# Kernel optimization log

Hardware: AMD Instinct MI355X
Metric: run time of the kernel (lower is better)

Reference implementation:

```python
import jax, jax.numpy as jnp
import numpy as np

N_EMBD = 1024
N_HEAD = 16
B, T = 4, 2048


def setup_inputs() -> dict:
    key = jax.random.key(0)
    ks = jax.random.split(key, 4)
    s = 1.0 / np.sqrt(N_EMBD)
    return {
        "x": jax.random.normal(ks[0], (B, T, N_EMBD), dtype=jnp.float32),
        "w_attn": jax.random.normal(ks[1], (N_EMBD, 3 * N_EMBD), dtype=jnp.float32) * s,
        "b_attn": jnp.zeros((3 * N_EMBD,), dtype=jnp.float32),
        "w_proj": jax.random.normal(ks[2], (N_EMBD, N_EMBD), dtype=jnp.float32) * s,
        "b_proj": jnp.zeros((N_EMBD,), dtype=jnp.float32),
    }


def reference(x, w_attn, b_attn, w_proj, b_proj):
    Bb, Tt, C = x.shape
    H = N_HEAD
    D = C // H  # head dim
    qkv = x @ w_attn + b_attn  # [B,T,3C]
    q, k, v = jnp.split(qkv, 3, axis=2)
    # [B,H,T,D]
    q = q.reshape(Bb, Tt, H, D).transpose(0, 2, 1, 3)
    k = k.reshape(Bb, Tt, H, D).transpose(0, 2, 1, 3)
    v = v.reshape(Bb, Tt, H, D).transpose(0, 2, 1, 3)
    scale = 1.0 / np.sqrt(D).astype(np.float32)
    attn = jnp.einsum("bhqd,bhkd->bhqk", q, k) * scale
    mask = jnp.tril(jnp.ones((Tt, Tt), dtype=bool))
    attn = jnp.where(mask, attn, jnp.float32(-jnp.inf))
    probs = jax.nn.softmax(attn, axis=-1)
    out = jnp.einsum("bhqk,bhkd->bhqd", probs, v)
    out = out.transpose(0, 2, 1, 3).reshape(Bb, Tt, C)
    return out @ w_proj + b_proj
```

## Files before the change

### kernel.cpp

```cpp
#include <hip/hip_runtime.h>
#include <hip/hip_bf16.h>


typedef float f32x4 __attribute__((ext_vector_type(4)));
typedef float f32x16 __attribute__((ext_vector_type(16)));
typedef short short8 __attribute__((ext_vector_type(8)));
typedef short short4v __attribute__((ext_vector_type(4)));

__device__ __forceinline__ short f2bf(float f) {
  union { __hip_bfloat16 h; short s; } u;
  u.h = __float2bfloat16(f);
  return u.s;
}

__device__ __forceinline__ void gl_lds16(const void* g, void* l) {
  __builtin_amdgcn_global_load_lds(
      (const __attribute__((address_space(1))) void*)g,
      (__attribute__((address_space(3))) void*)l, 16, 0, 0);
}

__global__ void prep(const float* __restrict__ x, const float* __restrict__ wa,
                     const float* __restrict__ wp, short* __restrict__ xb,
                     short* __restrict__ wat, short* __restrict__ wpt) {
  const int bid = blockIdx.x, tid = threadIdx.x;
  if (bid < 8192) {
    int i = (bid * 256 + tid) * 4;
    float4 v = *(const float4*)(x + i);
    short4v o;
    o[0] = f2bf(v.x); o[1] = f2bf(v.y); o[2] = f2bf(v.z); o[3] = f2bf(v.w);
    *(short4v*)(xb + i) = o;
    return;
  }
  __shared__ float tile[32][33];
  const float* in;
  short* out;
  int N, bx, by;
  if (bid < 11264) {
    int t = bid - 8192;
    in = wa; out = wat; N = 3072; bx = t % 96; by = t / 96;
  } else {
    int t = bid - 11264;
    in = wp; out = wpt; N = 1024; bx = t & 31; by = t >> 5;
  }
  int tx = tid & 31, ty = tid >> 5;
  int x0 = bx * 32, y0 = by * 32;
#pragma unroll
  for (int i = 0; i < 32; i += 8)
    tile[ty + i][tx] = in[(size_t)(y0 + ty + i) * N + x0 + tx];
  __syncthreads();
#pragma unroll
  for (int i = 0; i < 32; i += 8)
    out[(size_t)(x0 + ty + i) * 1024 + y0 + tx] = f2bf(tile[tx][ty + i]);
}


#define GEMM_BODY(A_, Bt_)                                                        \
  __shared__ __align__(16) short As[2][128 * 32];                                 \
  __shared__ __align__(16) short Bs[2][128 * 32];                                 \
  const int tid = threadIdx.x;                                                    \
  const int wv = tid >> 6;                                                        \
  const int wr = wv >> 1, wc = wv & 1;                                            \
  const int col = tid & 31, khalf = (tid >> 5) & 1;                               \
  const int m0 = blockIdx.y * 128, n0 = blockIdx.x * 128;                         \
  const int cc0 = tid, cc1 = tid + 256;                                           \
  const int row0 = cc0 >> 2, part0 = ((cc0 & 3) - ((cc0 >> 3) & 3)) & 3;          \
  const int row1 = cc1 >> 2, part1 = ((cc1 & 3) - ((cc1 >> 3) & 3)) & 3;          \
  const size_t ga0 = (size_t)(m0 + row0) * 1024 + part0 * 8;                      \
  const size_t ga1 = (size_t)(m0 + row1) * 1024 + part1 * 8;                      \
  const size_t gb0 = (size_t)(n0 + row0) * 1024 + part0 * 8;                      \
  const size_t gb1 = (size_t)(n0 + row1) * 1024 + part1 * 8;                      \
  f32x16 acc[2][2];                                                               \
  _Pragma("unroll") for (int i = 0; i < 2; ++i)                                   \
      _Pragma("unroll") for (int j = 0; j < 2; ++j)                               \
          acc[i][j] = (f32x16)(0.f);                                              \
  gl_lds16(A_ + ga0, (char*)As[0] + cc0 * 16);                                    \
  gl_lds16(A_ + ga1, (char*)As[0] + cc1 * 16);                                    \
  gl_lds16(Bt_ + gb0, (char*)Bs[0] + cc0 * 16);                                   \
  gl_lds16(Bt_ + gb1, (char*)Bs[0] + cc1 * 16);                                   \
  __syncthreads();                                                                \
  for (int kt = 0; kt < 32; ++kt) {                                               \
    if (kt + 1 < 32) {                                                            \
      const int k0 = (kt + 1) * 32;                                               \
      char* Ad = (char*)As[(kt + 1) & 1];                                         \
      char* Bd = (char*)Bs[(kt + 1) & 1];                                         \
      gl_lds16(A_ + ga0 + k0, Ad + cc0 * 16);                                     \
      gl_lds16(A_ + ga1 + k0, Ad + cc1 * 16);                                     \
      gl_lds16(Bt_ + gb0 + k0, Bd + cc0 * 16);                                    \
      gl_lds16(Bt_ + gb1 + k0, Bd + cc1 * 16);                                    \
    }                                                                             \
    const short* Ac = As[kt & 1];                                                 \
    const short* Bc = Bs[kt & 1];                                                 \
    short8 af[2][2], bf[2][2];                                                    \
    _Pragma("unroll") for (int i = 0; i < 2; ++i)                                 \
        _Pragma("unroll") for (int s = 0; s < 2; ++s) {                           \
          int pa = s * 2 + khalf;                                                 \
          int ra = wr * 64 + i * 32 + col;                                        \
          int rb = wc * 64 + i * 32 + col;                                        \
          af[i][s] = *(const short8*)&Ac[(ra * 4 + ((pa + (ra >> 1)) & 3)) * 8];  \
          bf[i][s] = *(const short8*)&Bc[(rb * 4 + ((pa + (rb >> 1)) & 3)) * 8];  \
        }                                                                         \
    _Pragma("unroll") for (int s = 0; s < 2; ++s)                                 \
        _Pragma("unroll") for (int i = 0; i < 2; ++i)                             \
            _Pragma("unroll") for (int j = 0; j < 2; ++j)                         \
                acc[i][j] = __builtin_amdgcn_mfma_f32_32x32x16_bf16(              \
                    af[i][s], bf[j][s], acc[i][j], 0, 0, 0);                      \
    __syncthreads();                                                              \
  }

__global__ __launch_bounds__(256, 2) void gemm_qkv(
    const short* __restrict__ A, const short* __restrict__ Bt,
    const float* __restrict__ bias, short* __restrict__ Qb,
    short* __restrict__ Kb, short* __restrict__ Vtb) {
  GEMM_BODY(A, Bt)
  const int rhalf = khalf * 4;
#pragma unroll
  for (int i = 0; i < 2; ++i) {
#pragma unroll
    for (int j = 0; j < 2; ++j) {
      int n = n0 + wc * 64 + j * 32 + col;
      int n2 = n & 1023;
      int hh = n2 >> 6, d = n2 & 63;
      float bv = bias[n];
      int mb = m0 + wr * 64 + i * 32 + rhalf;
      int bb = mb >> 11;
      int bh = (bb << 4) + hh;
      if (n < 2048) {
        const bool isq = n < 1024;
#pragma unroll
        for (int a = 0; a < 16; ++a) {
          int t = (mb + (a & 3) + 8 * (a >> 2)) & 2047;
          float o = acc[i][j][a] + bv;
          size_t idx = ((size_t)bh * 2048 + t) * 64 + d;
          if (isq)
            Qb[idx] = f2bf(o * 0.18033688f);
          else
            Kb[idx] = f2bf(o);
        }
      } else {
#pragma unroll
        for (int g = 0; g < 4; ++g) {
          int t = (mb + 8 * g) & 2047;
          short4v o;
#pragma unroll
          for (int r = 0; r < 4; ++r) o[r] = f2bf(acc[i][j][g * 4 + r] + bv);
          *(short4v*)&Vtb[((size_t)bh * 64 + d) * 2048 + t] = o;
        }
      }
    }
  }
}

__global__ __launch_bounds__(256, 2) void gemm_proj(
    const short* __restrict__ A, const short* __restrict__ Bt,
    const float* __restrict__ bias, float* __restrict__ out) {
  GEMM_BODY(A, Bt)
  const int rhalf = khalf * 4;
#pragma unroll
  for (int i = 0; i < 2; ++i) {
#pragma unroll
    for (int j = 0; j < 2; ++j) {
      int n = n0 + wc * 64 + j * 32 + col;
      float bv = bias[n];
      int mb = m0 + wr * 64 + i * 32 + rhalf;
#pragma unroll
      for (int a = 0; a < 16; ++a) {
        int m = mb + (a & 3) + 8 * (a >> 2);
        out[(size_t)m * 1024 + n] = acc[i][j][a] + bv;
      }
    }
  }
}

__global__ __launch_bounds__(256, 2) void flash_attn(
    const short* __restrict__ Qg_, const short* __restrict__ Kg_,
    const short* __restrict__ Vg_, short* __restrict__ Ob) {
  constexpr int STR = 72;
  __shared__ __align__(16) short Kl[2][64 * STR];
  __shared__ __align__(16) short Vl[2][64 * STR];
  const int tid = threadIdx.x;
  const int wv = tid >> 6, ln = tid & 15, quad = (tid & 63) >> 4;
  const int bh = blockIdx.x & 63;
  const int pair = blockIdx.x >> 6;
  const short* Qg = Qg_ + (size_t)bh * 2048 * 64;
  const short* Kg = Kg_ + (size_t)bh * 2048 * 64;
  const short* Vg = Vg_ + (size_t)bh * 64 * 2048;
  const int srow = tid >> 3, spart = tid & 7;
  const int bb = bh >> 4, hh = bh & 15;

  short8 kreg[2], vreg[2];

#define LOADKV(KT)                                                              \
  {                                                                             \
    const short* Kt = Kg + (size_t)(KT) * 64 * 64;                              \
    _Pragma("unroll") for (int i = 0; i < 2; ++i) {                             \
      kreg[i] = *(const short8*)(Kt + (size_t)(srow + i * 32) * 64 + spart * 8);\
      vreg[i] = *(const short8*)(Vg + (size_t)(srow + i * 32) * 2048 +          \
                                 (KT) * 64 + spart * 8);                        \
    }                                                                           \
  }
#define WRITEKV(BUF)                                                            \
  _Pragma("unroll") for (int i = 0; i < 2; ++i) {                               \
    *(short8*)&Kl[BUF][(srow + i * 32) * STR + spart * 8] = kreg[i];            \
    *(short8*)&Vl[BUF][(srow + i * 32) * STR + spart * 8] = vreg[i];            \
  }

#pragma unroll
  for (int it = 0; it < 2; ++it) {
    const int qt = it ? pair : (15 - pair);
    const int q0 = qt * 128;
    const int qbase = q0 + wv * 32;
    const int nkt = (q0 >> 6) + 2;

    short8 qf[2][2];
#pragma unroll
    for (int h = 0; h < 2; ++h)
#pragma unroll
      for (int ch = 0; ch < 2; ++ch)
        qf[h][ch] = *(const short8*)(Qg + (size_t)(qbase + h * 16 + ln) * 64 +
                                     ch * 32 + quad * 8);

    f32x4 Oacc[2][4];
#pragma unroll
    for (int h = 0; h < 2; ++h)
#pragma unroll
      for (int mt = 0; mt < 4; ++mt) Oacc[h][mt] = (f32x4){0.f, 0.f, 0.f, 0.f};
    float lpart[2] = {0.f, 0.f};

    LOADKV(0)
    __syncthreads();
    WRITEKV(0)
    LOADKV(1)

    for (int kt = 0; kt < nkt; ++kt) {
      __syncthreads();
      const short* Kcur = Kl[kt & 1];
      const short* Vcur = Vl[kt & 1];
      if (kt + 1 < nkt) {
        WRITEKV((kt + 1) & 1)
        if (kt + 2 < nkt) LOADKV(kt + 2)
      }

      if (kt * 64 <= qbase + 31) {
        f32x4 St[2][4];
#pragma unroll
        for (int h = 0; h < 2; ++h)
#pragma unroll
          for (int kb = 0; kb < 4; ++kb) St[h][kb] = (f32x4){0.f, 0.f, 0.f, 0.f};
        __builtin_amdgcn_s_setprio(1);
#pragma unroll
        for (int kb = 0; kb < 4; ++kb) {
          short8 ka0 = *(const short8*)&Kcur[(kb * 16 + ln) * STR + quad * 8];
          short8 ka1 = *(const short8*)&Kcur[(kb * 16 + ln) * STR + 32 + quad * 8];
#pragma unroll
          for (int h = 0; h < 2; ++h) {
            St[h][kb] = __builtin_amdgcn_mfma_f32_16x16x32_bf16(
                ka0, qf[h][0], St[h][kb], 0, 0, 0);
            St[h][kb] = __builtin_amdgcn_mfma_f32_16x16x32_bf16(
                ka1, qf[h][1], St[h][kb], 0, 0, 0);
          }
        }
        __builtin_amdgcn_s_setprio(0);

        short4v pf[2][4];
#pragma unroll
        for (int h = 0; h < 2; ++h) {
          float lp0 = 0.f, lp1 = 0.f;
          if (kt * 64 + 63 <= qbase + h * 16) {
#pragma unroll
            for (int kb = 0; kb < 4; ++kb) {
              float p[4];
#pragma unroll
              for (int r = 0; r < 4; ++r)
                p[r] = __builtin_amdgcn_exp2f(St[h][kb][r]);
              lp0 += p[0] + p[2];
              lp1 += p[1] + p[3];
              union { __hip_bfloat162 b2; unsigned u; } w0, w1;
              w0.b2 = __float22bfloat162_rn(make_float2(p[0], p[1]));
              w1.b2 = __float22bfloat162_rn(make_float2(p[2], p[3]));
              union { short4v s4; unsigned u2[2]; } m;
              m.u2[0] = w0.u; m.u2[1] = w1.u;
              pf[h][kb] = m.s4;
            }
          } else {
            const int qg = qbase + h * 16 + ln;
#pragma unroll
            for (int kb = 0; kb < 4; ++kb) {
              float p[4];
#pragma unroll
              for (int r = 0; r < 4; ++r) {
                int key = kt * 64 + kb * 16 + quad * 4 + r;
                float s = (key <= qg) ? St[h][kb][r] : -1e30f;
                p[r] = __builtin_amdgcn_exp2f(s);
              }
              lp0 += p[0] + p[2];
              lp1 += p[1] + p[3];
              union { __hip_bfloat162 b2; unsigned u; } w0, w1;
              w0.b2 = __float22bfloat162_rn(make_float2(p[0], p[1]));
              w1.b2 = __float22bfloat162_rn(make_float2(p[2], p[3]));
              union { short4v s4; unsigned u2[2]; } m;
              m.u2[0] = w0.u; m.u2[1] = w1.u;
              pf[h][kb] = m.s4;
            }
          }
          lpart[h] += lp0 + lp1;
        }

        __builtin_amdgcn_s_setprio(1);
#pragma unroll
        for (int kb = 0; kb < 4; ++kb)
#pragma unroll
          for (int mt = 0; mt < 4; ++mt) {
            short4v va =
                *(const short4v*)&Vcur[(mt * 16 + ln) * STR + kb * 16 + quad * 4];
#pragma unroll
            for (int h = 0; h < 2; ++h)
              Oacc[h][mt] = __builtin_amdgcn_mfma_f32_16x16x16bf16_1k(
                  va, pf[h][kb], Oacc[h][mt], 0, 0, 0);
          }
        __builtin_amdgcn_s_setprio(0);
      }
    }

#pragma unroll
    for (int h = 0; h < 2; ++h) {
      float l = lpart[h];
      l += __shfl_xor(l, 16);
      l += __shfl_xor(l, 32);
      float rl = 1.0f / l;
      int t = qbase + h * 16 + ln;
#pragma unroll
      for (int mt = 0; mt < 4; ++mt) {
        short4v o;
#pragma unroll
        for (int r = 0; r < 4; ++r) o[r] = f2bf(Oacc[h][mt][r] * rl);
        *(short4v*)(Ob + ((size_t)(bb * 2048 + t)) * 1024 + hh * 64 + mt * 16 +
                    quad * 4) = o;
      }
    }
  }
#undef LOADKV
#undef WRITEKV
}


extern "C" void kernel_launch(void* const* d_in, const int* in_sizes, int n_in,
                              void* d_out, int out_size, void* d_ws, size_t ws_size,
                              hipStream_t stream) {
  const float* x      = (const float*)d_in[0];
  const float* w_attn = (const float*)d_in[1];
  const float* b_attn = (const float*)d_in[2];
  const float* w_proj = (const float*)d_in[3];
  const float* b_proj = (const float*)d_in[4];
  float* out = (float*)d_out;
  char* ws = (char*)d_ws;

  short* xb  = (short*)(ws);
  short* wat = (short*)(ws + 16777216);
  short* wpt = (short*)(ws + 23068672);
  short* Qb  = (short*)(ws + 25165824);
  short* Kb  = (short*)(ws + 41943040);
  short* Vtb = (short*)(ws + 58720256);
  short* Ob  = (short*)(ws + 75497472);

  prep<<<12288, 256, 0, stream>>>(x, w_attn, w_proj, xb, wat, wpt);
  gemm_qkv<<<dim3(24, 64), 256, 0, stream>>>(xb, wat, b_attn, Qb, Kb, Vtb);
  flash_attn<<<512, 256, 0, stream>>>(Qb, Kb, Vtb, Ob);
  gemm_proj<<<dim3(8, 64), 256, 0, stream>>>(Ob, wpt, b_proj, out);
}
```

Baseline: 255.9 us.

## Drop LDS staging in flash attention, read K/V directly from global, one tile per block

Removes the shared-memory double-buffered K/V staging and the block barriers. Each wave now reads its K and V MFMA fragments straight from global memory, relying on L1/L2 to serve the reuse across the block's four waves. The paired-query-tile load balancing is replaced by one query tile per block, with twice as many blocks and a per-wave key-tile count. This removes LDS traffic and syncs, and lets lagging waves stop early. The cost is redundant global and cache loads, partly uncoalesced strided V reads, and possible load imbalance across blocks under the causal mask.

```diff
diff --git a/kernel.cpp b/kernel.cpp
--- a/kernel.cpp
+++ b/kernel.cpp
@@ -52,7 +52,6 @@
   for (int i = 0; i < 32; i += 8)
     out[(size_t)(x0 + ty + i) * 1024 + y0 + tx] = f2bf(tile[tx][ty + i]);
 }
-
 
 #define GEMM_BODY(A_, Bt_)                                                        \
   __shared__ __align__(16) short As[2][128 * 32];                                 \
@@ -174,172 +173,133 @@
 __global__ __launch_bounds__(256, 2) void flash_attn(
     const short* __restrict__ Qg_, const short* __restrict__ Kg_,
     const short* __restrict__ Vg_, short* __restrict__ Ob) {
-  constexpr int STR = 72;
-  __shared__ __align__(16) short Kl[2][64 * STR];
-  __shared__ __align__(16) short Vl[2][64 * STR];
   const int tid = threadIdx.x;
   const int wv = tid >> 6, ln = tid & 15, quad = (tid & 63) >> 4;
   const int bh = blockIdx.x & 63;
-  const int pair = blockIdx.x >> 6;
+  const int qt = 15 - (blockIdx.x >> 6);
   const short* Qg = Qg_ + (size_t)bh * 2048 * 64;
   const short* Kg = Kg_ + (size_t)bh * 2048 * 64;
   const short* Vg = Vg_ + (size_t)bh * 64 * 2048;
-  const int srow = tid >> 3, spart = tid & 7;
   const int bb = bh >> 4, hh = bh & 15;
 
-  short8 kreg[2], vreg[2];
-
-#define LOADKV(KT)                                                              \
-  {                                                                             \
-    const short* Kt = Kg + (size_t)(KT) * 64 * 64;                              \
-    _Pragma("unroll") for (int i = 0; i < 2; ++i) {                             \
-      kreg[i] = *(const short8*)(Kt + (size_t)(srow + i * 32) * 64 + spart * 8);\
-      vreg[i] = *(const short8*)(Vg + (size_t)(srow + i * 32) * 2048 +          \
-                                 (KT) * 64 + spart * 8);                        \
-    }                                                                           \
-  }
-#define WRITEKV(BUF)                                                            \
-  _Pragma("unroll") for (int i = 0; i < 2; ++i) {                               \
-    *(short8*)&Kl[BUF][(srow + i * 32) * STR + spart * 8] = kreg[i];            \
-    *(short8*)&Vl[BUF][(srow + i * 32) * STR + spart * 8] = vreg[i];            \
-  }
-
-#pragma unroll
-  for (int it = 0; it < 2; ++it) {
-    const int qt = it ? pair : (15 - pair);
-    const int q0 = qt * 128;
-    const int qbase = q0 + wv * 32;
-    const int nkt = (q0 >> 6) + 2;
-
-    short8 qf[2][2];
+  const int qbase = qt * 128 + wv * 32;
+  const int nkt = ((qbase + 31) >> 6) + 1;
+
+  short8 qf[2][2];
+#pragma unroll
+  for (int h = 0; h < 2; ++h)
+#pragma unroll
+    for (int ch = 0; ch < 2; ++ch)
+      qf[h][ch] = *(const short8*)(Qg + (size_t)(qbase + h * 16 + ln) * 64 +
+                                   ch * 32 + quad * 8);
+
+  f32x4 Oacc[2][4];
+#pragma unroll
+  for (int h = 0; h < 2; ++h)
+#pragma unroll
+    for (int mt = 0; mt < 4; ++mt) Oacc[h][mt] = (f32x4){0.f, 0.f, 0.f, 0.f};
+  float lpart[2] = {0.f, 0.f};
+
+  for (int kt = 0; kt < nkt; ++kt) {
+    const short* Kt = Kg + (size_t)kt * 64 * 64;
+    const short* Vt = Vg + kt * 64;
+
+    f32x4 St[2][4];
 #pragma unroll
     for (int h = 0; h < 2; ++h)
 #pragma unroll
-      for (int ch = 0; ch < 2; ++ch)
-        qf[h][ch] = *(const short8*)(Qg + (size_t)(qbase + h * 16 + ln) * 64 +
-                                     ch * 32 + quad * 8);
-
-    f32x4 Oacc[2][4];
-#pragma unroll
-    for (int h = 0; h < 2; ++h)
-#pragma unroll
-      for (int mt = 0; mt < 4; ++mt) Oacc[h][mt] = (f32x4){0.f, 0.f, 0.f, 0.f};
-    float lpart[2] = {0.f, 0.f};
-
-    LOADKV(0)
-    __syncthreads();
-    WRITEKV(0)
-    LOADKV(1)
-
-    for (int kt = 0; kt < nkt; ++kt) {
-      __syncthreads();
-      const short* Kcur = Kl[kt & 1];
-      const short* Vcur = Vl[kt & 1];
-      if (kt + 1 < nkt) {
-        WRITEKV((kt + 1) & 1)
-        if (kt + 2 < nkt) LOADKV(kt + 2)
-      }
-
-      if (kt * 64 <= qbase + 31) {
-        f32x4 St[2][4];
+      for (int kb = 0; kb < 4; ++kb) St[h][kb] = (f32x4){0.f, 0.f, 0.f, 0.f};
+    __builtin_amdgcn_s_setprio(1);
+#pragma unroll
+    for (int kb = 0; kb < 4; ++kb) {
+      short8 ka0 = *(const short8*)(Kt + (size_t)(kb * 16 + ln) * 64 + quad * 8);
+      short8 ka1 =
+          *(const short8*)(Kt + (size_t)(kb * 16 + ln) * 64 + 32 + quad * 8);
+#pragma unroll
+      for (int h = 0; h < 2; ++h) {
+        St[h][kb] = __builtin_amdgcn_mfma_f32_16x16x32_bf16(ka0, qf[h][0],
+                                                            St[h][kb], 0, 0, 0);
+        St[h][kb] = __builtin_amdgcn_mfma_f32_16x16x32_bf16(ka1, qf[h][1],
+                                                            St[h][kb], 0, 0, 0);
+      }
+    }
+    __builtin_amdgcn_s_setprio(0);
+
+    short4v pf[2][4];
+#pragma unroll
+    for (int h = 0; h < 2; ++h) {
+      float lp0 = 0.f, lp1 = 0.f;
+      if (kt * 64 + 63 <= qbase + h * 16) {
+#pragma unroll
+        for (int kb = 0; kb < 4; ++kb) {
+          float p[4];
+#pragma unroll
+          for (int r = 0; r < 4; ++r)
+            p[r] = __builtin_amdgcn_exp2f(St[h][kb][r]);
+          lp0 += p[0] + p[2];
+          lp1 += p[1] + p[3];
+          union { __hip_bfloat162 b2; unsigned u; } w0, w1;
+          w0.b2 = __float22bfloat162_rn(make_float2(p[0], p[1]));
+          w1.b2 = __float22bfloat162_rn(make_float2(p[2], p[3]));
+          union { short4v s4; unsigned u2[2]; } m;
+          m.u2[0] = w0.u; m.u2[1] = w1.u;
+          pf[h][kb] = m.s4;
+        }
+      } else {
+        const int qg = qbase + h * 16 + ln;
+#pragma unroll
+        for (int kb = 0; kb < 4; ++kb) {
+          float p[4];
+#pragma unroll
+          for (int r = 0; r < 4; ++r) {
+            int key = kt * 64 + kb * 16 + quad * 4 + r;
+            float s = (key <= qg) ? St[h][kb][r] : -1e30f;
+            p[r] = __builtin_amdgcn_exp2f(s);
+          }
+          lp0 += p[0] + p[2];
+          lp1 += p[1] + p[3];
+          union { __hip_bfloat162 b2; unsigned u; } w0, w1;
+          w0.b2 = __float22bfloat162_rn(make_float2(p[0], p[1]));
+          w1.b2 = __float22bfloat162_rn(make_float2(p[2], p[3]));
+          union { short4v s4; unsigned u2[2]; } m;
+          m.u2[0] = w0.u; m.u2[1] = w1.u;
+          pf[h][kb] = m.s4;
+        }
+      }
+      lpart[h] += lp0 + lp1;
+    }
+
+    __builtin_amdgcn_s_setprio(1);
+#pragma unroll
+    for (int kb = 0; kb < 4; ++kb)
+#pragma unroll
+      for (int mt = 0; mt < 4; ++mt) {
+        short4v va = *(const short4v*)(Vt + (size_t)(mt * 16 + ln) * 2048 +
+                                       kb * 16 + quad * 4);
 #pragma unroll
         for (int h = 0; h < 2; ++h)
-#pragma unroll
-          for (int kb = 0; kb < 4; ++kb) St[h][kb] = (f32x4){0.f, 0.f, 0.f, 0.f};
-        __builtin_amdgcn_s_setprio(1);
-#pragma unroll
-        for (int kb = 0; kb < 4; ++kb) {
-          short8 ka0 = *(const short8*)&Kcur[(kb * 16 + ln) * STR + quad * 8];
-          short8 ka1 = *(const short8*)&Kcur[(kb * 16 + ln) * STR + 32 + quad * 8];
-#pragma unroll
-          for (int h = 0; h < 2; ++h) {
-            St[h][kb] = __builtin_amdgcn_mfma_f32_16x16x32_bf16(
-                ka0, qf[h][0], St[h][kb], 0, 0, 0);
-            St[h][kb] = __builtin_amdgcn_mfma_f32_16x16x32_bf16(
-                ka1, qf[h][1], St[h][kb], 0, 0, 0);
-          }
-        }
-        __builtin_amdgcn_s_setprio(0);
-
-        short4v pf[2][4];
-#pragma unroll
-        for (int h = 0; h < 2; ++h) {
-          float lp0 = 0.f, lp1 = 0.f;
-          if (kt * 64 + 63 <= qbase + h * 16) {
-#pragma unroll
-            for (int kb = 0; kb < 4; ++kb) {
-              float p[4];
-#pragma unroll
-              for (int r = 0; r < 4; ++r)
-                p[r] = __builtin_amdgcn_exp2f(St[h][kb][r]);
-              lp0 += p[0] + p[2];
-              lp1 += p[1] + p[3];
-              union { __hip_bfloat162 b2; unsigned u; } w0, w1;
-              w0.b2 = __float22bfloat162_rn(make_float2(p[0], p[1]));
-              w1.b2 = __float22bfloat162_rn(make_float2(p[2], p[3]));
-              union { short4v s4; unsigned u2[2]; } m;
-              m.u2[0] = w0.u; m.u2[1] = w1.u;
-              pf[h][kb] = m.s4;
-            }
-          } else {
-            const int qg = qbase + h * 16 + ln;
-#pragma unroll
-            for (int kb = 0; kb < 4; ++kb) {
-              float p[4];
-#pragma unroll
-              for (int r = 0; r < 4; ++r) {
-                int key = kt * 64 + kb * 16 + quad * 4 + r;
-                float s = (key <= qg) ? St[h][kb][r] : -1e30f;
-                p[r] = __builtin_amdgcn_exp2f(s);
-              }
-              lp0 += p[0] + p[2];
-              lp1 += p[1] + p[3];
-              union { __hip_bfloat162 b2; unsigned u; } w0, w1;
-              w0.b2 = __float22bfloat162_rn(make_float2(p[0], p[1]));
-              w1.b2 = __float22bfloat162_rn(make_float2(p[2], p[3]));
-              union { short4v s4; unsigned u2[2]; } m;
-              m.u2[0] = w0.u; m.u2[1] = w1.u;
-              pf[h][kb] = m.s4;
-            }
-          }
-          lpart[h] += lp0 + lp1;
-        }
-
-        __builtin_amdgcn_s_setprio(1);
-#pragma unroll
-        for (int kb = 0; kb < 4; ++kb)
-#pragma unroll
-          for (int mt = 0; mt < 4; ++mt) {
-            short4v va =
-                *(const short4v*)&Vcur[(mt * 16 + ln) * STR + kb * 16 + quad * 4];
-#pragma unroll
-            for (int h = 0; h < 2; ++h)
-              Oacc[h][mt] = __builtin_amdgcn_mfma_f32_16x16x16bf16_1k(
-                  va, pf[h][kb], Oacc[h][mt], 0, 0, 0);
-          }
-        __builtin_amdgcn_s_setprio(0);
-      }
-    }
-
-#pragma unroll
-    for (int h = 0; h < 2; ++h) {
-      float l = lpart[h];
-      l += __shfl_xor(l, 16);
-      l += __shfl_xor(l, 32);
-      float rl = 1.0f / l;
-      int t = qbase + h * 16 + ln;
-#pragma unroll
-      for (int mt = 0; mt < 4; ++mt) {
-        short4v o;
-#pragma unroll
-        for (int r = 0; r < 4; ++r) o[r] = f2bf(Oacc[h][mt][r] * rl);
-        *(short4v*)(Ob + ((size_t)(bb * 2048 + t)) * 1024 + hh * 64 + mt * 16 +
-                    quad * 4) = o;
-      }
-    }
-  }
-#undef LOADKV
-#undef WRITEKV
+          Oacc[h][mt] = __builtin_amdgcn_mfma_f32_16x16x16bf16_1k(
+              va, pf[h][kb], Oacc[h][mt], 0, 0, 0);
+      }
+    __builtin_amdgcn_s_setprio(0);
+  }
+
+#pragma unroll
+  for (int h = 0; h < 2; ++h) {
+    float l = lpart[h];
+    l += __shfl_xor(l, 16);
+    l += __shfl_xor(l, 32);
+    float rl = 1.0f / l;
+    int t = qbase + h * 16 + ln;
+#pragma unroll
+    for (int mt = 0; mt < 4; ++mt) {
+      short4v o;
+#pragma unroll
+      for (int r = 0; r < 4; ++r) o[r] = f2bf(Oacc[h][mt][r] * rl);
+      *(short4v*)(Ob + ((size_t)(bb * 2048 + t)) * 1024 + hh * 64 + mt * 16 +
+                  quad * 4) = o;
+    }
+  }
 }
 
 
@@ -364,6 +324,6 @@
 
   prep<<<12288, 256, 0, stream>>>(x, w_attn, w_proj, xb, wat, wpt);
   gemm_qkv<<<dim3(24, 64), 256, 0, stream>>>(xb, wat, b_attn, Qb, Kb, Vtb);
-  flash_attn<<<512, 256, 0, stream>>>(Qb, Kb, Vtb, Ob);
+  flash_attn<<<1024, 256, 0, stream>>>(Qb, Kb, Vtb, Ob);
   gemm_proj<<<dim3(8, 64), 256, 0, stream>>>(Ob, wpt, b_proj, out);
 }
```

Measured after the change: 404.0 us. +57.8%, slower.
